# Performance work log

Hardware: AMD Instinct MI355X
Metric: run time of the kernel (lower is better)

Reference implementation:

```python
import jax, jax.numpy as jnp
import numpy as np

B, H, W, C = 4, 64, 64, 256
D = C // 8  # out_channels // queries_ratio = 32


def setup_inputs() -> dict:
    key = jax.random.key(0)
    ks = jax.random.split(key, 8)
    s_in = 1.0 / np.sqrt(C)  # he_normal-ish scale for 1x1 convs
    s_d = 1.0 / np.sqrt(D)
    return {
        "x": jax.random.normal(ks[0], (B, H, W, C), dtype=jnp.float32),
        "Wk": jax.random.normal(ks[1], (C, D), dtype=jnp.float32) * s_in,
        "bk": jnp.zeros((D,), dtype=jnp.float32),
        "Wq": jax.random.normal(ks[2], (C, D), dtype=jnp.float32) * s_in,
        "bq": jnp.zeros((D,), dtype=jnp.float32),
        "Wv": jax.random.normal(ks[3], (C, D), dtype=jnp.float32) * s_in,
        "bv": jnp.zeros((D,), dtype=jnp.float32),
        "Wo": jax.random.normal(ks[4], (D, C), dtype=jnp.float32) * s_d,
        "bo": jnp.zeros((C,), dtype=jnp.float32),
        "gamma": jax.random.normal(ks[5], (1,), dtype=jnp.float32) * 0.1,
    }


def reference(x, Wk, bk, Wq, bq, Wv, bv, Wo, bo, gamma):
    b, h, w, c = x.shape
    n = h * w
    xf = x.reshape(b, n, c)  # flatten spatial -> [B, N, C]
    # 1x1 convs == per-position channel matmuls
    k = xf @ Wk + bk  # [B, N, D]
    q = xf @ Wq + bq  # [B, N, D]
    v = xf @ Wv + bv  # [B, N, D]
    energy = jnp.einsum('bnd,bmd->bnm', q, k)  # [B, N, N] (no scaling, as in source)
    attn = jax.nn.softmax(energy, axis=-1)
    feat = jnp.einsum('bnm,bmd->bnd', attn, v)  # [B, N, D]
    out = feat @ Wo + bo  # 1x1 output conv -> [B, N, C]
    out = gamma[0] * out + xf  # gamma scale + identity shortcut (C_in == C_out)
    return out.reshape(b, h, w, c)
```

## Files before the change

### kernel.cpp

```cpp
#include <hip/hip_runtime.h>
#include <hip/hip_bf16.h>
#include <hip/hip_fp16.h>


#define BB 4
#define NN 4096
#define CC 256
#define DD 32
#define LOG2E 1.44269504088896340736f
#define THR2 11.0f

typedef _Float16 half_t;
typedef _Float16 half2_t __attribute__((ext_vector_type(2)));
typedef _Float16 half4_t __attribute__((ext_vector_type(4)));
typedef _Float16 half8_t __attribute__((ext_vector_type(8)));
typedef float f32x4 __attribute__((ext_vector_type(4)));

#define MFMA_QK(a, b, c) __builtin_amdgcn_mfma_f32_16x16x32_f16(a, b, c, 0, 0, 0)
#define MFMA_PV(a, b, c) __builtin_amdgcn_mfma_f32_16x16x16f16(a, b, c, 0, 0, 0)

static __device__ inline float fexp2(float x) {
#if __has_builtin(__builtin_amdgcn_exp2f)
    return __builtin_amdgcn_exp2f(x);
#else
    return exp2f(x);
#endif
}

__global__ __launch_bounds__(512) void proj_kernel(
    const float* __restrict__ x,
    const float* __restrict__ Wk, const float* __restrict__ bk,
    const float* __restrict__ Wq, const float* __restrict__ bq,
    const float* __restrict__ Wv, const float* __restrict__ bv,
    half_t* __restrict__ k_ws, half_t* __restrict__ q_ws, half_t* __restrict__ vT2)
{
    __shared__ half_t xs16[64][264];
    __shared__ half_t Wt[96][264];

    const int t = threadIdx.x;
    const int xcd = blockIdx.x & 7, slot = blockIdx.x >> 3;
    const int bb = xcd >> 1;
    const int c64 = (slot << 1) | (xcd & 1);
    const int row0 = bb * NN + c64 * 64;

    const float4* x4 = reinterpret_cast<const float4*>(x) + (size_t)row0 * 64;
    for (int idx = t; idx < 64 * 64; idx += 512) {
        int r = idx >> 6, c4 = idx & 63;
        float4 v = x4[r * 64 + c4];
        half4_t h;
        h[0] = (half_t)v.x; h[1] = (half_t)v.y; h[2] = (half_t)v.z; h[3] = (half_t)v.w;
        *reinterpret_cast<half4_t*>(&xs16[r][c4 * 4]) = h;
    }

    for (int idx = t; idx < 3072; idx += 512) {
        int cp = idx & 127;
        int rest = idx >> 7;
        int d4 = (rest & 7) * 4;
        int mat = rest >> 3;
        const float* Wm = (mat == 0) ? Wk : ((mat == 1) ? Wq : Wv);
        const float sc = (mat == 1) ? LOG2E : 1.0f;
        float4 w0 = *reinterpret_cast<const float4*>(Wm + (2 * cp) * DD + d4);
        float4 w1 = *reinterpret_cast<const float4*>(Wm + (2 * cp + 1) * DD + d4);
        int rbase = mat * 32 + d4;
        half2_t h;
        h[0] = (half_t)(w0.x * sc); h[1] = (half_t)(w1.x * sc);
        *reinterpret_cast<half2_t*>(&Wt[rbase + 0][2 * cp]) = h;
        h[0] = (half_t)(w0.y * sc); h[1] = (half_t)(w1.y * sc);
        *reinterpret_cast<half2_t*>(&Wt[rbase + 1][2 * cp]) = h;
        h[0] = (half_t)(w0.z * sc); h[1] = (half_t)(w1.z * sc);
        *reinterpret_cast<half2_t*>(&Wt[rbase + 2][2 * cp]) = h;
        h[0] = (half_t)(w0.w * sc); h[1] = (half_t)(w1.w * sc);
        *reinterpret_cast<half2_t*>(&Wt[rbase + 3][2 * cp]) = h;
    }
    __syncthreads();

    const int w = t >> 6, lane = t & 63;
    const int c = lane & 15, g = lane >> 4;
    const int rt = w >> 1;
    const int ct0 = (w & 1) * 3;

    f32x4 acc[3];
#pragma unroll
    for (int j = 0; j < 3; ++j) acc[j] = (f32x4){0.f, 0.f, 0.f, 0.f};

#pragma unroll
    for (int kk = 0; kk < 8; ++kk) {
        const int k0 = kk * 32 + g * 8;
        half8_t bfrag = *reinterpret_cast<const half8_t*>(&xs16[rt * 16 + c][k0]);
#pragma unroll
        for (int j = 0; j < 3; ++j) {
            half8_t afrag = *reinterpret_cast<const half8_t*>(&Wt[(ct0 + j) * 16 + c][k0]);
            acc[j] = MFMA_QK(afrag, bfrag, acc[j]);
        }
    }

    const int grow = row0 + rt * 16 + c;
#pragma unroll
    for (int j = 0; j < 3; ++j) {
        const int ct = ct0 + j;
        const int mat = ct >> 1;
        const float* bm = (mat == 0) ? bk : ((mat == 1) ? bq : bv);
        float4 bb4 = *reinterpret_cast<const float4*>(bm + (ct & 1) * 16 + g * 4);
        if (mat < 2) {
            const float bsc = (mat == 1) ? LOG2E : 1.0f;
            half_t* dst = (mat == 0) ? k_ws : q_ws;
            half4_t h;
            h[0] = (half_t)(acc[j][0] + bb4.x * bsc);
            h[1] = (half_t)(acc[j][1] + bb4.y * bsc);
            h[2] = (half_t)(acc[j][2] + bb4.z * bsc);
            h[3] = (half_t)(acc[j][3] + bb4.w * bsc);
            *reinterpret_cast<half4_t*>(dst + (size_t)grow * DD + (ct & 1) * 16 + g * 4) = h;
        } else {
            const size_t tbase = ((size_t)(row0 >> 4) + rt) * 512;
            const int d0 = (ct & 1) * 16 + g * 4;
            vT2[tbase + (size_t)(d0 + 0) * 16 + c] = (half_t)(acc[j][0] + bb4.x);
            vT2[tbase + (size_t)(d0 + 1) * 16 + c] = (half_t)(acc[j][1] + bb4.y);
            vT2[tbase + (size_t)(d0 + 2) * 16 + c] = (half_t)(acc[j][2] + bb4.z);
            vT2[tbase + (size_t)(d0 + 3) * 16 + c] = (half_t)(acc[j][3] + bb4.w);
        }
    }
}

__global__ __launch_bounds__(512) void attn_kernel(
    const half_t* __restrict__ k_ws, const half_t* __restrict__ q_ws,
    const half_t* __restrict__ vT2,
    const float* __restrict__ x, const float* __restrict__ Wo,
    const float* __restrict__ bo, const float* __restrict__ gamma,
    float* __restrict__ out)
{
    __shared__ float acc_l[8][64][33];
    __shared__ float m_l[8][4][16];
    __shared__ float s_l[8][4][16];
    __shared__ half_t feat_h[64 * 40];
    __shared__ half_t woT[256 * 40];

    const int tid = threadIdx.x;
    const int w = tid >> 6, lane = tid & 63;
    const int q = lane & 15, g = lane >> 4;
    const int xcd = blockIdx.x & 7, slot = blockIdx.x >> 3;
    const int b = xcd >> 1;
    const int qb = (slot << 1) | (xcd & 1);
    const int q0 = qb * 64;

#pragma unroll
    for (int it = 0; it < 16; ++it) {
        int idx = tid + it * 512;
        int c = idx & 255, d = idx >> 8;
        woT[c * 40 + d] = (half_t)Wo[d * CC + c];
    }

    half8_t qf[4];
#pragma unroll
    for (int t = 0; t < 4; ++t)
        qf[t] = *reinterpret_cast<const half8_t*>(
            q_ws + (size_t)(b * NN + q0 + t * 16 + q) * DD + g * 8);

    float m[4], ssum[4];
    f32x4 accd0[4], accd1[4];
#pragma unroll
    for (int t = 0; t < 4; ++t) {
        m[t] = -3.0e38f; ssum[t] = 0.f;
        accd0[t] = (f32x4){0.f, 0.f, 0.f, 0.f};
        accd1[t] = (f32x4){0.f, 0.f, 0.f, 0.f};
    }

    const half_t* kbase = k_ws + ((size_t)b * NN + q) * DD + g * 8;
    const half_t* vb = vT2 + (size_t)b * 256 * 512 + q * 16 + g * 4;

    const int ktbase = w * 32;

    half8_t kc0 = *reinterpret_cast<const half8_t*>(kbase + (size_t)(ktbase + 0) * 16 * DD);
    half8_t kc1 = *reinterpret_cast<const half8_t*>(kbase + (size_t)(ktbase + 1) * 16 * DD);
    half4_t va0 = *reinterpret_cast<const half4_t*>(vb + (size_t)(ktbase + 0) * 512);
    half4_t va1 = *reinterpret_cast<const half4_t*>(vb + (size_t)(ktbase + 0) * 512 + 256);
    half4_t vc0 = *reinterpret_cast<const half4_t*>(vb + (size_t)(ktbase + 1) * 512);
    half4_t vc1 = *reinterpret_cast<const half4_t*>(vb + (size_t)(ktbase + 1) * 512 + 256);

    for (int it = 0; it < 16; ++it) {
        const int kt = ktbase + it * 2;
        const int ktn = (it < 15) ? (kt + 2) : kt;

        half8_t kn0 = *reinterpret_cast<const half8_t*>(kbase + (size_t)(ktn + 0) * 16 * DD);
        half8_t kn1 = *reinterpret_cast<const half8_t*>(kbase + (size_t)(ktn + 1) * 16 * DD);
        half4_t wa0 = *reinterpret_cast<const half4_t*>(vb + (size_t)(ktn + 0) * 512);
        half4_t wa1 = *reinterpret_cast<const half4_t*>(vb + (size_t)(ktn + 0) * 512 + 256);
        half4_t wc0 = *reinterpret_cast<const half4_t*>(vb + (size_t)(ktn + 1) * 512);
        half4_t wc1 = *reinterpret_cast<const half4_t*>(vb + (size_t)(ktn + 1) * 512 + 256);

        f32x4 z = {0.f, 0.f, 0.f, 0.f};
        f32x4 s0[4], s1[4];
#pragma unroll
        for (int t = 0; t < 4; ++t) {
            s0[t] = MFMA_QK(kc0, qf[t], z);
            s1[t] = MFMA_QK(kc1, qf[t], z);
        }

        float tmax[4];
        bool need = false;
#pragma unroll
        for (int t = 0; t < 4; ++t) {
            float t0 = fmaxf(fmaxf(s0[t][0], s0[t][1]), fmaxf(s0[t][2], s0[t][3]));
            float t1 = fmaxf(fmaxf(s1[t][0], s1[t][1]), fmaxf(s1[t][2], s1[t][3]));
            tmax[t] = fmaxf(t0, t1);
            need = need || (tmax[t] > m[t] + THR2);
        }

        if (__any(need)) {
#pragma unroll
            for (int t = 0; t < 4; ++t) {
                float rmax = tmax[t];
                rmax = fmaxf(rmax, __shfl_xor(rmax, 16));
                rmax = fmaxf(rmax, __shfl_xor(rmax, 32));
                float mn = fmaxf(m[t], rmax);
                float sc = fexp2(m[t] - mn);
                ssum[t] *= sc;
                accd0[t] *= sc;
                accd1[t] *= sc;
                m[t] = mn;
            }
        }

#pragma unroll
        for (int t = 0; t < 4; ++t) {
            float p00 = fexp2(s0[t][0] - m[t]), p01 = fexp2(s0[t][1] - m[t]);
            float p02 = fexp2(s0[t][2] - m[t]), p03 = fexp2(s0[t][3] - m[t]);
            float p10 = fexp2(s1[t][0] - m[t]), p11 = fexp2(s1[t][1] - m[t]);
            float p12 = fexp2(s1[t][2] - m[t]), p13 = fexp2(s1[t][3] - m[t]);
            ssum[t] += ((p00 + p01) + (p02 + p03)) + ((p10 + p11) + (p12 + p13));

            half4_t pf0, pf1;
            pf0[0] = (half_t)p00; pf0[1] = (half_t)p01; pf0[2] = (half_t)p02; pf0[3] = (half_t)p03;
            pf1[0] = (half_t)p10; pf1[1] = (half_t)p11; pf1[2] = (half_t)p12; pf1[3] = (half_t)p13;

            accd0[t] = MFMA_PV(va0, pf0, accd0[t]);
            accd1[t] = MFMA_PV(va1, pf0, accd1[t]);
            accd0[t] = MFMA_PV(vc0, pf1, accd0[t]);
            accd1[t] = MFMA_PV(vc1, pf1, accd1[t]);
        }

        kc0 = kn0; kc1 = kn1;
        va0 = wa0; va1 = wa1; vc0 = wc0; vc1 = wc1;
    }

#pragma unroll
    for (int t = 0; t < 4; ++t) {
        ssum[t] += __shfl_xor(ssum[t], 16);
        ssum[t] += __shfl_xor(ssum[t], 32);
    }

    if (lane < 16) {
#pragma unroll
        for (int t = 0; t < 4; ++t) { m_l[w][t][lane] = m[t]; s_l[w][t][lane] = ssum[t]; }
    }
#pragma unroll
    for (int t = 0; t < 4; ++t)
#pragma unroll
        for (int i = 0; i < 4; ++i) {
            acc_l[w][lane][t * 8 + i] = accd0[t][i];
            acc_l[w][lane][t * 8 + 4 + i] = accd1[t][i];
        }
    __syncthreads();

    if (w < 4) {
        const int t = w;
        float M = m_l[0][t][q];
#pragma unroll
        for (int ww = 1; ww < 8; ++ww) M = fmaxf(M, m_l[ww][t][q]);
        float SS = 0.f;
        float f[8] = {0.f, 0.f, 0.f, 0.f, 0.f, 0.f, 0.f, 0.f};
#pragma unroll
        for (int ww = 0; ww < 8; ++ww) {
            float sc = fexp2(m_l[ww][t][q] - M);
            SS += s_l[ww][t][q] * sc;
#pragma unroll
            for (int i = 0; i < 8; ++i) f[i] += acc_l[ww][lane][t * 8 + i] * sc;
        }
        float inv = 1.0f / SS;
        half4_t h0, h1;
#pragma unroll
        for (int i = 0; i < 4; ++i) { h0[i] = (half_t)(f[i] * inv); h1[i] = (half_t)(f[4 + i] * inv); }
        *reinterpret_cast<half4_t*>(&feat_h[(t * 16 + q) * 40 + g * 4]) = h0;
        *reinterpret_cast<half4_t*>(&feat_h[(t * 16 + q) * 40 + 16 + g * 4]) = h1;
    }
    __syncthreads();

    const float gam = gamma[0];
#pragma unroll
    for (int j = 0; j < 2; ++j) {
        const int ct = w * 2 + j;
        half8_t kfe = *reinterpret_cast<const half8_t*>(&woT[(ct * 16 + q) * 40 + g * 8]);
        float4 bb4 = *reinterpret_cast<const float4*>(bo + ct * 16 + g * 4);
#pragma unroll
        for (int rt = 0; rt < 4; ++rt) {
            half8_t qfe = *reinterpret_cast<const half8_t*>(&feat_h[(rt * 16 + q) * 40 + g * 8]);
            f32x4 z = {0.f, 0.f, 0.f, 0.f};
            f32x4 o = MFMA_QK(kfe, qfe, z);
            const size_t base = ((size_t)b * NN + q0 + rt * 16 + q) * CC + ct * 16 + g * 4;
            float4 xv = *reinterpret_cast<const float4*>(x + base);
            float4 ov;
            ov.x = gam * (o[0] + bb4.x) + xv.x;
            ov.y = gam * (o[1] + bb4.y) + xv.y;
            ov.z = gam * (o[2] + bb4.z) + xv.z;
            ov.w = gam * (o[3] + bb4.w) + xv.w;
            *reinterpret_cast<float4*>(out + base) = ov;
        }
    }
}

extern "C" void kernel_launch(void* const* d_in, const int* in_sizes, int n_in,
                              void* d_out, int out_size, void* d_ws, size_t ws_size,
                              hipStream_t stream) {
    const float* x  = (const float*)d_in[0];
    const float* Wk = (const float*)d_in[1];
    const float* bk = (const float*)d_in[2];
    const float* Wq = (const float*)d_in[3];
    const float* bq = (const float*)d_in[4];
    const float* Wv = (const float*)d_in[5];
    const float* bv = (const float*)d_in[6];
    const float* Wo = (const float*)d_in[7];
    const float* bo = (const float*)d_in[8];
    const float* gamma = (const float*)d_in[9];
    float* out = (float*)d_out;

    half_t* k_ws  = (half_t*)d_ws;
    half_t* q_ws  = k_ws + (size_t)BB * NN * DD;
    half_t* vT2   = q_ws + (size_t)BB * NN * DD;

    proj_kernel<<<256, 512, 0, stream>>>(x, Wk, bk, Wq, bq, Wv, bv, k_ws, q_ws, vT2);
    attn_kernel<<<256, 512, 0, stream>>>(k_ws, q_ws, vT2, x, Wo, bo, gamma, out);
}
```

Baseline: 38.89 us.

## Split attention over keys with LDS-staged K/V and separate combine kernel

Restructures attention into a split-K partial kernel, where each block handles 256 queries over a quarter of the keys, plus a combine kernel that merges the partial softmax states and applies the output projection. K and V tiles are staged into double-buffered LDS with global_load_lds, and V is laid out so each lane reads one contiguous 8-half vector. The goal is to share K/V loads across more queries per block and hide load latency. The cost is an extra kernel launch and a round trip of fp32 partial results through global memory.

```diff
diff --git a/kernel.cpp b/kernel.cpp
--- a/kernel.cpp
+++ b/kernel.cpp
@@ -9,6 +9,9 @@
 #define DD 32
 #define LOG2E 1.44269504088896340736f
 #define THR2 11.0f
+#define NROW (BB * NN)
+#define KSPLIT 4
+#define NCH 16
 
 typedef _Float16 half_t;
 typedef _Float16 half2_t __attribute__((ext_vector_type(2)));
@@ -27,12 +30,18 @@
 #endif
 }
 
+static __device__ __forceinline__ void stage16(const void* g, void* l) {
+    __builtin_amdgcn_global_load_lds(
+        (const __attribute__((address_space(1))) void*)g,
+        (__attribute__((address_space(3))) void*)l, 16, 0, 0);
+}
+
 __global__ __launch_bounds__(512) void proj_kernel(
     const float* __restrict__ x,
     const float* __restrict__ Wk, const float* __restrict__ bk,
     const float* __restrict__ Wq, const float* __restrict__ bq,
     const float* __restrict__ Wv, const float* __restrict__ bv,
-    half_t* __restrict__ k_ws, half_t* __restrict__ q_ws, half_t* __restrict__ vT2)
+    half_t* __restrict__ k_ws, half_t* __restrict__ q_ws, half_t* __restrict__ vT3)
 {
     __shared__ half_t xs16[64][264];
     __shared__ half_t Wt[96][264];
@@ -111,36 +120,148 @@
             h[3] = (half_t)(acc[j][3] + bb4.w * bsc);
             *reinterpret_cast<half4_t*>(dst + (size_t)grow * DD + (ct & 1) * 16 + g * 4) = h;
         } else {
-            const size_t tbase = ((size_t)(row0 >> 4) + rt) * 512;
+            const size_t tbase = (size_t)(grow >> 4) * 512;
             const int d0 = (ct & 1) * 16 + g * 4;
-            vT2[tbase + (size_t)(d0 + 0) * 16 + c] = (half_t)(acc[j][0] + bb4.x);
-            vT2[tbase + (size_t)(d0 + 1) * 16 + c] = (half_t)(acc[j][1] + bb4.y);
-            vT2[tbase + (size_t)(d0 + 2) * 16 + c] = (half_t)(acc[j][2] + bb4.z);
-            vT2[tbase + (size_t)(d0 + 3) * 16 + c] = (half_t)(acc[j][3] + bb4.w);
-        }
-    }
-}
-
-__global__ __launch_bounds__(512) void attn_kernel(
+            float bbi[4] = {bb4.x, bb4.y, bb4.z, bb4.w};
+#pragma unroll
+            for (int i = 0; i < 4; ++i) {
+                int d = d0 + i;
+                int l = ((c >> 2) << 4) | (d & 15);
+                int h = l * 8 + ((d >> 4) << 2) + (c & 3);
+                vT3[tbase + h] = (half_t)(acc[j][i] + bbi[i]);
+            }
+        }
+    }
+}
+
+__global__ __launch_bounds__(512) void attn_partial(
     const half_t* __restrict__ k_ws, const half_t* __restrict__ q_ws,
-    const half_t* __restrict__ vT2,
+    const half_t* __restrict__ vT3,
+    float* __restrict__ pm, float* __restrict__ ps, float* __restrict__ pO)
+{
+    __shared__ half_t kbuf[2][4][512];
+    __shared__ half_t vbuf[2][4][512];
+
+    const int tid = threadIdx.x;
+    const int w = tid >> 6, lane = tid & 63;
+    const int q = lane & 15, g = lane >> 4;
+    const int qu = blockIdx.x >> 4;
+    const int b = (blockIdx.x >> 2) & 3;
+    const int ks = blockIdx.x & 3;
+    const int r0 = b * NN + qu * 256;
+
+    half8_t qf0 = *reinterpret_cast<const half8_t*>(
+        q_ws + (size_t)(r0 + (2 * w + 0) * 16 + q) * DD + g * 8);
+    half8_t qf1 = *reinterpret_cast<const half8_t*>(
+        q_ws + (size_t)(r0 + (2 * w + 1) * 16 + q) * DD + g * 8);
+
+    float m[2] = {-3.0e38f, -3.0e38f}, ssum[2] = {0.f, 0.f};
+    f32x4 accd0[2], accd1[2];
+#pragma unroll
+    for (int j = 0; j < 2; ++j) {
+        accd0[j] = (f32x4){0.f, 0.f, 0.f, 0.f};
+        accd1[j] = (f32x4){0.f, 0.f, 0.f, 0.f};
+    }
+
+    const int ktile0 = b * 256 + ks * 64;
+    const char* kb = (const char*)k_ws;
+    const char* vb = (const char*)vT3;
+    const int ksrc_off = q * 64 + g * 16;
+
+    {
+        const size_t nt = (size_t)(ktile0 + (w & 3)) * 1024;
+        if (w < 4) stage16(kb + nt + ksrc_off, &kbuf[0][w][0]);
+        else       stage16(vb + nt + lane * 16, &vbuf[0][w - 4][0]);
+    }
+
+    for (int ch = 0; ch < NCH; ++ch) {
+        __syncthreads();
+        const int cb = ch & 1;
+        if (ch + 1 < NCH) {
+            const size_t nt = (size_t)(ktile0 + (ch + 1) * 4 + (w & 3)) * 1024;
+            if (w < 4) stage16(kb + nt + ksrc_off, &kbuf[cb ^ 1][w][0]);
+            else       stage16(vb + nt + lane * 16, &vbuf[cb ^ 1][w - 4][0]);
+        }
+
+#pragma unroll
+        for (int tile = 0; tile < 4; ++tile) {
+            half8_t kf = *reinterpret_cast<const half8_t*>(&kbuf[cb][tile][lane * 8]);
+            half8_t vv = *reinterpret_cast<const half8_t*>(&vbuf[cb][tile][lane * 8]);
+
+            f32x4 z = {0.f, 0.f, 0.f, 0.f};
+            f32x4 s0 = MFMA_QK(kf, qf0, z);
+            f32x4 s1 = MFMA_QK(kf, qf1, z);
+
+            float t0 = fmaxf(fmaxf(s0[0], s0[1]), fmaxf(s0[2], s0[3]));
+            float t1 = fmaxf(fmaxf(s1[0], s1[1]), fmaxf(s1[2], s1[3]));
+            bool need = (t0 > m[0] + THR2) || (t1 > m[1] + THR2);
+            if (__any(need)) {
+                float r0m = fmaxf(t0, __shfl_xor(t0, 16));
+                r0m = fmaxf(r0m, __shfl_xor(r0m, 32));
+                float r1m = fmaxf(t1, __shfl_xor(t1, 16));
+                r1m = fmaxf(r1m, __shfl_xor(r1m, 32));
+                float mn0 = fmaxf(m[0], r0m), mn1 = fmaxf(m[1], r1m);
+                float sc0 = fexp2(m[0] - mn0), sc1 = fexp2(m[1] - mn1);
+                ssum[0] *= sc0; ssum[1] *= sc1;
+                accd0[0] *= sc0; accd1[0] *= sc0;
+                accd0[1] *= sc1; accd1[1] *= sc1;
+                m[0] = mn0; m[1] = mn1;
+            }
+
+            float p00 = fexp2(s0[0] - m[0]), p01 = fexp2(s0[1] - m[0]);
+            float p02 = fexp2(s0[2] - m[0]), p03 = fexp2(s0[3] - m[0]);
+            float p10 = fexp2(s1[0] - m[1]), p11 = fexp2(s1[1] - m[1]);
+            float p12 = fexp2(s1[2] - m[1]), p13 = fexp2(s1[3] - m[1]);
+            ssum[0] += (p00 + p01) + (p02 + p03);
+            ssum[1] += (p10 + p11) + (p12 + p13);
+
+            half4_t pf0, pf1;
+            pf0[0] = (half_t)p00; pf0[1] = (half_t)p01; pf0[2] = (half_t)p02; pf0[3] = (half_t)p03;
+            pf1[0] = (half_t)p10; pf1[1] = (half_t)p11; pf1[2] = (half_t)p12; pf1[3] = (half_t)p13;
+
+            half4_t va0 = __builtin_shufflevector(vv, vv, 0, 1, 2, 3);
+            half4_t va1 = __builtin_shufflevector(vv, vv, 4, 5, 6, 7);
+
+            accd0[0] = MFMA_PV(va0, pf0, accd0[0]);
+            accd1[0] = MFMA_PV(va1, pf0, accd1[0]);
+            accd0[1] = MFMA_PV(va0, pf1, accd0[1]);
+            accd1[1] = MFMA_PV(va1, pf1, accd1[1]);
+        }
+    }
+
+#pragma unroll
+    for (int j = 0; j < 2; ++j) {
+        ssum[j] += __shfl_xor(ssum[j], 16);
+        ssum[j] += __shfl_xor(ssum[j], 32);
+    }
+
+#pragma unroll
+    for (int j = 0; j < 2; ++j) {
+        const int r = r0 + (2 * w + j) * 16 + q;
+        if (lane < 16) {
+            pm[(size_t)ks * NROW + r0 + (2 * w + j) * 16 + lane] = m[j];
+            ps[(size_t)ks * NROW + r0 + (2 * w + j) * 16 + lane] = ssum[j];
+        }
+        float* po = pO + ((size_t)ks * NROW + r) * 32;
+        *reinterpret_cast<f32x4*>(po + g * 4) = accd0[j];
+        *reinterpret_cast<f32x4*>(po + 16 + g * 4) = accd1[j];
+    }
+}
+
+__global__ __launch_bounds__(512) void attn_combine(
+    const float* __restrict__ pm, const float* __restrict__ ps,
+    const float* __restrict__ pO,
     const float* __restrict__ x, const float* __restrict__ Wo,
     const float* __restrict__ bo, const float* __restrict__ gamma,
     float* __restrict__ out)
 {
-    __shared__ float acc_l[8][64][33];
-    __shared__ float m_l[8][4][16];
-    __shared__ float s_l[8][4][16];
     __shared__ half_t feat_h[64 * 40];
     __shared__ half_t woT[256 * 40];
 
     const int tid = threadIdx.x;
-    const int w = tid >> 6, lane = tid & 63;
-    const int q = lane & 15, g = lane >> 4;
-    const int xcd = blockIdx.x & 7, slot = blockIdx.x >> 3;
-    const int b = xcd >> 1;
-    const int qb = (slot << 1) | (xcd & 1);
+    const int b = blockIdx.x >> 6, qb = blockIdx.x & 63;
     const int q0 = qb * 64;
+    const int r0 = b * NN + q0;
 
 #pragma unroll
     for (int it = 0; it < 16; ++it) {
@@ -149,141 +270,33 @@
         woT[c * 40 + d] = (half_t)Wo[d * CC + c];
     }
 
-    half8_t qf[4];
-#pragma unroll
-    for (int t = 0; t < 4; ++t)
-        qf[t] = *reinterpret_cast<const half8_t*>(
-            q_ws + (size_t)(b * NN + q0 + t * 16 + q) * DD + g * 8);
-
-    float m[4], ssum[4];
-    f32x4 accd0[4], accd1[4];
-#pragma unroll
-    for (int t = 0; t < 4; ++t) {
-        m[t] = -3.0e38f; ssum[t] = 0.f;
-        accd0[t] = (f32x4){0.f, 0.f, 0.f, 0.f};
-        accd1[t] = (f32x4){0.f, 0.f, 0.f, 0.f};
-    }
-
-    const half_t* kbase = k_ws + ((size_t)b * NN + q) * DD + g * 8;
-    const half_t* vb = vT2 + (size_t)b * 256 * 512 + q * 16 + g * 4;
-
-    const int ktbase = w * 32;
-
-    half8_t kc0 = *reinterpret_cast<const half8_t*>(kbase + (size_t)(ktbase + 0) * 16 * DD);
-    half8_t kc1 = *reinterpret_cast<const half8_t*>(kbase + (size_t)(ktbase + 1) * 16 * DD);
-    half4_t va0 = *reinterpret_cast<const half4_t*>(vb + (size_t)(ktbase + 0) * 512);
-    half4_t va1 = *reinterpret_cast<const half4_t*>(vb + (size_t)(ktbase + 0) * 512 + 256);
-    half4_t vc0 = *reinterpret_cast<const half4_t*>(vb + (size_t)(ktbase + 1) * 512);
-    half4_t vc1 = *reinterpret_cast<const half4_t*>(vb + (size_t)(ktbase + 1) * 512 + 256);
-
-    for (int it = 0; it < 16; ++it) {
-        const int kt = ktbase + it * 2;
-        const int ktn = (it < 15) ? (kt + 2) : kt;
-
-        half8_t kn0 = *reinterpret_cast<const half8_t*>(kbase + (size_t)(ktn + 0) * 16 * DD);
-        half8_t kn1 = *reinterpret_cast<const half8_t*>(kbase + (size_t)(ktn + 1) * 16 * DD);
-        half4_t wa0 = *reinterpret_cast<const half4_t*>(vb + (size_t)(ktn + 0) * 512);
-        half4_t wa1 = *reinterpret_cast<const half4_t*>(vb + (size_t)(ktn + 0) * 512 + 256);
-        half4_t wc0 = *reinterpret_cast<const half4_t*>(vb + (size_t)(ktn + 1) * 512);
-        half4_t wc1 = *reinterpret_cast<const half4_t*>(vb + (size_t)(ktn + 1) * 512 + 256);
-
-        f32x4 z = {0.f, 0.f, 0.f, 0.f};
-        f32x4 s0[4], s1[4];
-#pragma unroll
-        for (int t = 0; t < 4; ++t) {
-            s0[t] = MFMA_QK(kc0, qf[t], z);
-            s1[t] = MFMA_QK(kc1, qf[t], z);
-        }
-
-        float tmax[4];
-        bool need = false;
-#pragma unroll
-        for (int t = 0; t < 4; ++t) {
-            float t0 = fmaxf(fmaxf(s0[t][0], s0[t][1]), fmaxf(s0[t][2], s0[t][3]));
-            float t1 = fmaxf(fmaxf(s1[t][0], s1[t][1]), fmaxf(s1[t][2], s1[t][3]));
-            tmax[t] = fmaxf(t0, t1);
-            need = need || (tmax[t] > m[t] + THR2);
-        }
-
-        if (__any(need)) {
-#pragma unroll
-            for (int t = 0; t < 4; ++t) {
-                float rmax = tmax[t];
-                rmax = fmaxf(rmax, __shfl_xor(rmax, 16));
-                rmax = fmaxf(rmax, __shfl_xor(rmax, 32));
-                float mn = fmaxf(m[t], rmax);
-                float sc = fexp2(m[t] - mn);
-                ssum[t] *= sc;
-                accd0[t] *= sc;
-                accd1[t] *= sc;
-                m[t] = mn;
-            }
-        }
-
-#pragma unroll
-        for (int t = 0; t < 4; ++t) {
-            float p00 = fexp2(s0[t][0] - m[t]), p01 = fexp2(s0[t][1] - m[t]);
-            float p02 = fexp2(s0[t][2] - m[t]), p03 = fexp2(s0[t][3] - m[t]);
-            float p10 = fexp2(s1[t][0] - m[t]), p11 = fexp2(s1[t][1] - m[t]);
-            float p12 = fexp2(s1[t][2] - m[t]), p13 = fexp2(s1[t][3] - m[t]);
-            ssum[t] += ((p00 + p01) + (p02 + p03)) + ((p10 + p11) + (p12 + p13));
-
-            half4_t pf0, pf1;
-            pf0[0] = (half_t)p00; pf0[1] = (half_t)p01; pf0[2] = (half_t)p02; pf0[3] = (half_t)p03;
-            pf1[0] = (half_t)p10; pf1[1] = (half_t)p11; pf1[2] = (half_t)p12; pf1[3] = (half_t)p13;
-
-            accd0[t] = MFMA_PV(va0, pf0, accd0[t]);
-            accd1[t] = MFMA_PV(va1, pf0, accd1[t]);
-            accd0[t] = MFMA_PV(vc0, pf1, accd0[t]);
-            accd1[t] = MFMA_PV(vc1, pf1, accd1[t]);
-        }
-
-        kc0 = kn0; kc1 = kn1;
-        va0 = wa0; va1 = wa1; vc0 = wc0; vc1 = wc1;
-    }
-
-#pragma unroll
-    for (int t = 0; t < 4; ++t) {
-        ssum[t] += __shfl_xor(ssum[t], 16);
-        ssum[t] += __shfl_xor(ssum[t], 32);
-    }
-
-    if (lane < 16) {
-#pragma unroll
-        for (int t = 0; t < 4; ++t) { m_l[w][t][lane] = m[t]; s_l[w][t][lane] = ssum[t]; }
-    }
-#pragma unroll
-    for (int t = 0; t < 4; ++t)
-#pragma unroll
-        for (int i = 0; i < 4; ++i) {
-            acc_l[w][lane][t * 8 + i] = accd0[t][i];
-            acc_l[w][lane][t * 8 + 4 + i] = accd1[t][i];
-        }
+    {
+        const int r = tid >> 3, d4 = (tid & 7) * 4;
+        const int gr = r0 + r;
+        float mv[4];
+        float M = -3.0e38f;
+#pragma unroll
+        for (int k = 0; k < KSPLIT; ++k) {
+            mv[k] = pm[(size_t)k * NROW + gr];
+            M = fmaxf(M, mv[k]);
+        }
+        float S = 0.f;
+        f32x4 f = {0.f, 0.f, 0.f, 0.f};
+#pragma unroll
+        for (int k = 0; k < KSPLIT; ++k) {
+            float wgt = fexp2(mv[k] - M);
+            S += ps[(size_t)k * NROW + gr] * wgt;
+            f32x4 p = *reinterpret_cast<const f32x4*>(pO + ((size_t)k * NROW + gr) * 32 + d4);
+            f += p * wgt;
+        }
+        float inv = 1.0f / S;
+#pragma unroll
+        for (int i = 0; i < 4; ++i) feat_h[r * 40 + d4 + i] = (half_t)(f[i] * inv);
+    }
     __syncthreads();
 
-    if (w < 4) {
-        const int t = w;
-        float M = m_l[0][t][q];
-#pragma unroll
-        for (int ww = 1; ww < 8; ++ww) M = fmaxf(M, m_l[ww][t][q]);
-        float SS = 0.f;
-        float f[8] = {0.f, 0.f, 0.f, 0.f, 0.f, 0.f, 0.f, 0.f};
-#pragma unroll
-        for (int ww = 0; ww < 8; ++ww) {
-            float sc = fexp2(m_l[ww][t][q] - M);
-            SS += s_l[ww][t][q] * sc;
-#pragma unroll
-            for (int i = 0; i < 8; ++i) f[i] += acc_l[ww][lane][t * 8 + i] * sc;
-        }
-        float inv = 1.0f / SS;
-        half4_t h0, h1;
-#pragma unroll
-        for (int i = 0; i < 4; ++i) { h0[i] = (half_t)(f[i] * inv); h1[i] = (half_t)(f[4 + i] * inv); }
-        *reinterpret_cast<half4_t*>(&feat_h[(t * 16 + q) * 40 + g * 4]) = h0;
-        *reinterpret_cast<half4_t*>(&feat_h[(t * 16 + q) * 40 + 16 + g * 4]) = h1;
-    }
-    __syncthreads();
-
+    const int w = tid >> 6, lane = tid & 63;
+    const int q = lane & 15, g = lane >> 4;
     const float gam = gamma[0];
 #pragma unroll
     for (int j = 0; j < 2; ++j) {
@@ -322,10 +335,14 @@
     const float* gamma = (const float*)d_in[9];
     float* out = (float*)d_out;
 
-    half_t* k_ws  = (half_t*)d_ws;
-    half_t* q_ws  = k_ws + (size_t)BB * NN * DD;
-    half_t* vT2   = q_ws + (size_t)BB * NN * DD;
-
-    proj_kernel<<<256, 512, 0, stream>>>(x, Wk, bk, Wq, bq, Wv, bv, k_ws, q_ws, vT2);
-    attn_kernel<<<256, 512, 0, stream>>>(k_ws, q_ws, vT2, x, Wo, bo, gamma, out);
-}
+    half_t* k_ws = (half_t*)d_ws;
+    half_t* q_ws = k_ws + (size_t)BB * NN * DD;
+    half_t* vT3  = q_ws + (size_t)BB * NN * DD;
+    float*  pm   = (float*)(vT3 + (size_t)BB * NN * DD);
+    float*  ps   = pm + (size_t)KSPLIT * NROW;
+    float*  pO   = ps + (size_t)KSPLIT * NROW;
+
+    proj_kernel<<<256, 512, 0, stream>>>(x, Wk, bk, Wq, bq, Wv, bv, k_ws, q_ws, vT3);
+    attn_partial<<<256, 512, 0, stream>>>(k_ws, q_ws, vT3, pm, ps, pO);
+    attn_combine<<<256, 512, 0, stream>>>(pm, ps, pO, x, Wo, bo, gamma, out);
+}
```

After: 49.29 us. +26.7%, slower.

## Store V in FP8 E4M3 with per-lane packed layout for single 16-byte loads

Applied to the files above, without the earlier changes.

V projections are now written as FP8 E4M3 instead of FP16, in a layout pre-arranged so each lane fetches all its V operands for an iteration with one 16-byte load. The loads are converted back to half in registers before the PV MFMAs. This halves V traffic and cuts the load instruction count per iteration. In exchange it adds conversion ALU work in the inner loop and reduces V precision to 3 mantissa bits, which may loosen accuracy against the reference.

```diff
diff --git a/kernel.cpp b/kernel.cpp
--- a/kernel.cpp
+++ b/kernel.cpp
@@ -1,6 +1,7 @@
 #include <hip/hip_runtime.h>
 #include <hip/hip_bf16.h>
 #include <hip/hip_fp16.h>
+#include <hip/hip_fp8.h>
 
 
 #define BB 4
@@ -27,12 +28,24 @@
 #endif
 }
 
+static __device__ __forceinline__ half4_t fp8x4_to_half4(unsigned int v) {
+    __half2_raw lo = __hip_cvt_fp8x2_to_halfraw2((__hip_fp8x2_storage_t)(v & 0xffffu), __HIP_E4M3);
+    __half2_raw hi = __hip_cvt_fp8x2_to_halfraw2((__hip_fp8x2_storage_t)(v >> 16), __HIP_E4M3);
+    half4_t r;
+    r[0] = *reinterpret_cast<_Float16*>(&lo.x);
+    r[1] = *reinterpret_cast<_Float16*>(&lo.y);
+    r[2] = *reinterpret_cast<_Float16*>(&hi.x);
+    r[3] = *reinterpret_cast<_Float16*>(&hi.y);
+    return r;
+}
+
 __global__ __launch_bounds__(512) void proj_kernel(
     const float* __restrict__ x,
     const float* __restrict__ Wk, const float* __restrict__ bk,
     const float* __restrict__ Wq, const float* __restrict__ bq,
     const float* __restrict__ Wv, const float* __restrict__ bv,
-    half_t* __restrict__ k_ws, half_t* __restrict__ q_ws, half_t* __restrict__ vT2)
+    half_t* __restrict__ k_ws, half_t* __restrict__ q_ws,
+    unsigned char* __restrict__ vT4)
 {
     __shared__ half_t xs16[64][264];
     __shared__ half_t Wt[96][264];
@@ -101,6 +114,7 @@
         const int mat = ct >> 1;
         const float* bm = (mat == 0) ? bk : ((mat == 1) ? bq : bv);
         float4 bb4 = *reinterpret_cast<const float4*>(bm + (ct & 1) * 16 + g * 4);
+        const int d0 = (ct & 1) * 16 + g * 4;
         if (mat < 2) {
             const float bsc = (mat == 1) ? LOG2E : 1.0f;
             half_t* dst = (mat == 0) ? k_ws : q_ws;
@@ -109,21 +123,28 @@
             h[1] = (half_t)(acc[j][1] + bb4.y * bsc);
             h[2] = (half_t)(acc[j][2] + bb4.z * bsc);
             h[3] = (half_t)(acc[j][3] + bb4.w * bsc);
-            *reinterpret_cast<half4_t*>(dst + (size_t)grow * DD + (ct & 1) * 16 + g * 4) = h;
+            *reinterpret_cast<half4_t*>(dst + (size_t)grow * DD + d0) = h;
         } else {
-            const size_t tbase = ((size_t)(row0 >> 4) + rt) * 512;
-            const int d0 = (ct & 1) * 16 + g * 4;
-            vT2[tbase + (size_t)(d0 + 0) * 16 + c] = (half_t)(acc[j][0] + bb4.x);
-            vT2[tbase + (size_t)(d0 + 1) * 16 + c] = (half_t)(acc[j][1] + bb4.y);
-            vT2[tbase + (size_t)(d0 + 2) * 16 + c] = (half_t)(acc[j][2] + bb4.z);
-            vT2[tbase + (size_t)(d0 + 3) * 16 + c] = (half_t)(acc[j][3] + bb4.w);
+            const int n = grow;
+            const size_t pbase = (size_t)(n >> 5) * 1024;
+            const int ko = n & 31;
+            const int lanehi = ((ko >> 2) & 3) * 16;
+            const int bytebase = ((ko >> 4) << 3) + (ko & 3);
+            float vals[4] = {acc[j][0] + bb4.x, acc[j][1] + bb4.y,
+                             acc[j][2] + bb4.z, acc[j][3] + bb4.w};
+#pragma unroll
+            for (int i = 0; i < 4; ++i) {
+                int d = d0 + i;
+                __hip_fp8_e4m3 f(vals[i]);
+                vT4[pbase + (size_t)(lanehi + (d & 15)) * 16 + bytebase + ((d >> 4) << 2)] = f.__x;
+            }
         }
     }
 }
 
 __global__ __launch_bounds__(512) void attn_kernel(
     const half_t* __restrict__ k_ws, const half_t* __restrict__ q_ws,
-    const half_t* __restrict__ vT2,
+    const unsigned char* __restrict__ vT4,
     const float* __restrict__ x, const float* __restrict__ Wo,
     const float* __restrict__ bo, const float* __restrict__ gamma,
     float* __restrict__ out)
@@ -165,27 +186,23 @@
     }
 
     const half_t* kbase = k_ws + ((size_t)b * NN + q) * DD + g * 8;
-    const half_t* vb = vT2 + (size_t)b * 256 * 512 + q * 16 + g * 4;
+    const unsigned char* vb4 = vT4 + (size_t)b * 131072 + (size_t)lane * 16
+                             + (size_t)w * 16 * 1024;
 
     const int ktbase = w * 32;
 
     half8_t kc0 = *reinterpret_cast<const half8_t*>(kbase + (size_t)(ktbase + 0) * 16 * DD);
     half8_t kc1 = *reinterpret_cast<const half8_t*>(kbase + (size_t)(ktbase + 1) * 16 * DD);
-    half4_t va0 = *reinterpret_cast<const half4_t*>(vb + (size_t)(ktbase + 0) * 512);
-    half4_t va1 = *reinterpret_cast<const half4_t*>(vb + (size_t)(ktbase + 0) * 512 + 256);
-    half4_t vc0 = *reinterpret_cast<const half4_t*>(vb + (size_t)(ktbase + 1) * 512);
-    half4_t vc1 = *reinterpret_cast<const half4_t*>(vb + (size_t)(ktbase + 1) * 512 + 256);
+    uint4 vvc = *reinterpret_cast<const uint4*>(vb4);
 
     for (int it = 0; it < 16; ++it) {
         const int kt = ktbase + it * 2;
-        const int ktn = (it < 15) ? (kt + 2) : kt;
+        const int itn = (it < 15) ? (it + 1) : it;
+        const int ktn = ktbase + itn * 2;
 
         half8_t kn0 = *reinterpret_cast<const half8_t*>(kbase + (size_t)(ktn + 0) * 16 * DD);
         half8_t kn1 = *reinterpret_cast<const half8_t*>(kbase + (size_t)(ktn + 1) * 16 * DD);
-        half4_t wa0 = *reinterpret_cast<const half4_t*>(vb + (size_t)(ktn + 0) * 512);
-        half4_t wa1 = *reinterpret_cast<const half4_t*>(vb + (size_t)(ktn + 0) * 512 + 256);
-        half4_t wc0 = *reinterpret_cast<const half4_t*>(vb + (size_t)(ktn + 1) * 512);
-        half4_t wc1 = *reinterpret_cast<const half4_t*>(vb + (size_t)(ktn + 1) * 512 + 256);
+        uint4 vvn = *reinterpret_cast<const uint4*>(vb4 + (size_t)itn * 1024);
 
         f32x4 z = {0.f, 0.f, 0.f, 0.f};
         f32x4 s0[4], s1[4];
@@ -220,6 +237,11 @@
             }
         }
 
+        half4_t va0 = fp8x4_to_half4(vvc.x);
+        half4_t va1 = fp8x4_to_half4(vvc.y);
+        half4_t vc0 = fp8x4_to_half4(vvc.z);
+        half4_t vc1 = fp8x4_to_half4(vvc.w);
+
 #pragma unroll
         for (int t = 0; t < 4; ++t) {
             float p00 = fexp2(s0[t][0] - m[t]), p01 = fexp2(s0[t][1] - m[t]);
@@ -238,8 +260,7 @@
             accd1[t] = MFMA_PV(vc1, pf1, accd1[t]);
         }
 
-        kc0 = kn0; kc1 = kn1;
-        va0 = wa0; va1 = wa1; vc0 = wc0; vc1 = wc1;
+        kc0 = kn0; kc1 = kn1; vvc = vvn;
     }
 
 #pragma unroll
@@ -322,10 +343,10 @@
     const float* gamma = (const float*)d_in[9];
     float* out = (float*)d_out;
 
-    half_t* k_ws  = (half_t*)d_ws;
-    half_t* q_ws  = k_ws + (size_t)BB * NN * DD;
-    half_t* vT2   = q_ws + (size_t)BB * NN * DD;
-
-    proj_kernel<<<256, 512, 0, stream>>>(x, Wk, bk, Wq, bq, Wv, bv, k_ws, q_ws, vT2);
-    attn_kernel<<<256, 512, 0, stream>>>(k_ws, q_ws, vT2, x, Wo, bo, gamma, out);
-}
+    half_t* k_ws = (half_t*)d_ws;
+    half_t* q_ws = k_ws + (size_t)BB * NN * DD;
+    unsigned char* vT4 = (unsigned char*)(q_ws + (size_t)BB * NN * DD);
+
+    proj_kernel<<<256, 512, 0, stream>>>(x, Wk, bk, Wq, bq, Wv, bv, k_ws, q_ws, vT4);
+    attn_kernel<<<256, 512, 0, stream>>>(k_ws, q_ws, vT4, x, Wo, bo, gamma, out);
+}
```

Measured after the change: 65.28 us. 1.68x slower.
